# Kernel tuning notes

Measured on AMD Instinct MI355X. Metric: run time of the kernel, lower is better.

## Reference

```python
import jax, jax.numpy as jnp
import numpy as np

G = 7          # grid size
OBJ_P = 0.3    # fraction of cells containing an object


def _to_xyxy(x, y, w, h, m, n):
    # x pairs with grid index m (dim 2), y with n (dim 3), per the original loop
    cx = (x + m) / G
    cy = (y + n) / G
    return cx - w / 2, cy - h / 2, cx + w / 2, cy + h / 2


def _iou(b1, b2):
    x1a, y1a, x2a, y2a = b1
    x1b, y1b, x2b, y2b = b2
    iw = jnp.maximum(jnp.minimum(x2a, x2b) - jnp.maximum(x1a, x1b), 0.0)
    ih = jnp.maximum(jnp.minimum(y2a, y2b) - jnp.maximum(y1a, y1b), 0.0)
    inter = iw * ih
    a1 = (x2a - x1a) * (y2a - y1a)
    a2 = (x2b - x1b) * (y2b - y1b)
    union = a1 + a2 - inter
    return jnp.where(inter > 0, inter / union, 0.0)


def setup_inputs() -> dict:
    key = jax.random.key(0)
    k1, k2, k3 = jax.random.split(key, 3)
    B = 32768
    pred = jax.random.uniform(k1, (B, 30, G, G), dtype=jnp.float32)
    labels = jax.random.uniform(k2, (B, 30, G, G), dtype=jnp.float32)
    obj_mask = jax.random.bernoulli(k3, OBJ_P, (B, G, G)).astype(jnp.float32)
    labels = labels.at[:, 4].set(obj_mask)
    return {"pred": pred, "labels": labels}


def reference(pred, labels):
    B = pred.shape[0]
    m = jnp.arange(G, dtype=pred.dtype)[:, None]   # dim 2
    n = jnp.arange(G, dtype=pred.dtype)[None, :]   # dim 3

    obj = labels[:, 4] == 1.0                       # (B,G,G)

    box1 = _to_xyxy(pred[:, 0], pred[:, 1], pred[:, 2], pred[:, 3], m, n)
    box2 = _to_xyxy(pred[:, 5], pred[:, 6], pred[:, 7], pred[:, 8], m, n)
    boxg = _to_xyxy(labels[:, 0], labels[:, 1], labels[:, 2], labels[:, 3], m, n)

    iou1 = _iou(box1, boxg)
    iou2 = _iou(box2, boxg)
    resp1 = iou1 >= iou2

    coor1 = 5.0 * (jnp.sum((pred[:, 0:2] - labels[:, 0:2]) ** 2, axis=1)
                   + jnp.sum((jnp.sqrt(pred[:, 2:4]) - jnp.sqrt(labels[:, 2:4])) ** 2, axis=1))
    coor2 = 5.0 * (jnp.sum((pred[:, 5:7] - labels[:, 5:7]) ** 2, axis=1)
                   + jnp.sum((jnp.sqrt(pred[:, 7:9]) - jnp.sqrt(labels[:, 7:9])) ** 2, axis=1))

    loss_b1 = coor1 + (pred[:, 4] - iou1) ** 2 + 0.5 * (pred[:, 9] - iou2) ** 2
    loss_b2 = coor2 + (pred[:, 9] - iou2) ** 2 + 0.5 * (pred[:, 4] - iou1) ** 2

    cls = jnp.sum((pred[:, 10:] - labels[:, 10:]) ** 2, axis=1)

    obj_loss = jnp.where(resp1, loss_b1, loss_b2) + cls
    noobj_loss = 0.5 * (pred[:, 4] ** 2 + pred[:, 9] ** 2)

    total = jnp.sum(jnp.where(obj, obj_loss, noobj_loss))
    return total / B
```

## Files before the change

kernel.cpp:

```cpp
#include <hip/hip_runtime.h>


#define GRID 7
#define NCH 30
#define CPI (GRID * GRID)
#define FPI (NCH * CPI)
#define IPB 4
#define BLK 256
#define CELLS_PB (IPB * CPI)
#define F_PB (IPB * FPI)
#define F4_PB (F_PB / 4)
#define FALLBACK_NBLK 2048

typedef const __attribute__((address_space(1))) void gvoid_t;
typedef __attribute__((address_space(3))) void lvoid_t;

__device__ __forceinline__ float iou_xyxy(float x1a, float y1a, float x2a, float y2a,
                                          float x1b, float y1b, float x2b, float y2b) {
    float iw = fmaxf(fminf(x2a, x2b) - fmaxf(x1a, x1b), 0.0f);
    float ih = fmaxf(fminf(y2a, y2b) - fmaxf(y1a, y1b), 0.0f);
    float inter = iw * ih;
    float a1 = (x2a - x1a) * (y2a - y1a);
    float a2 = (x2b - x1b) * (y2b - y1b);
    float uni = a1 + a2 - inter;
    return inter > 0.0f ? inter / uni : 0.0f;
}

__device__ __forceinline__ float cell_loss(const float* __restrict__ pb,
                                           const float* __restrict__ lb,
                                           float fm, float fn) {
    float p0 = pb[0 * CPI], p1 = pb[1 * CPI], p2 = pb[2 * CPI], p3 = pb[3 * CPI];
    float p4 = pb[4 * CPI], p5 = pb[5 * CPI], p6 = pb[6 * CPI], p7 = pb[7 * CPI];
    float p8 = pb[8 * CPI], p9 = pb[9 * CPI];
    float l0 = lb[0 * CPI], l1 = lb[1 * CPI], l2 = lb[2 * CPI], l3 = lb[3 * CPI];
    float lobj = lb[4 * CPI];
    float l5 = lb[5 * CPI], l6 = lb[6 * CPI], l7 = lb[7 * CPI], l8 = lb[8 * CPI];

    float cls = 0.0f;
    #pragma unroll
    for (int c = 10; c < NCH; ++c) {
        float d = pb[c * CPI] - lb[c * CPI];
        cls += d * d;
    }

    const float inv_g = 1.0f / (float)GRID;

    float cx = (p0 + fm) * inv_g, cy = (p1 + fn) * inv_g;
    float b1x1 = cx - p2 * 0.5f, b1y1 = cy - p3 * 0.5f;
    float b1x2 = cx + p2 * 0.5f, b1y2 = cy + p3 * 0.5f;
    cx = (p5 + fm) * inv_g; cy = (p6 + fn) * inv_g;
    float b2x1 = cx - p7 * 0.5f, b2y1 = cy - p8 * 0.5f;
    float b2x2 = cx + p7 * 0.5f, b2y2 = cy + p8 * 0.5f;
    cx = (l0 + fm) * inv_g; cy = (l1 + fn) * inv_g;
    float gx1 = cx - l2 * 0.5f, gy1 = cy - l3 * 0.5f;
    float gx2 = cx + l2 * 0.5f, gy2 = cy + l3 * 0.5f;

    float iou1 = iou_xyxy(b1x1, b1y1, b1x2, b1y2, gx1, gy1, gx2, gy2);
    float iou2 = iou_xyxy(b2x1, b2y1, b2x2, b2y2, gx1, gy1, gx2, gy2);
    bool resp1 = iou1 >= iou2;

    float dx = p0 - l0, dy = p1 - l1;
    float dw = sqrtf(p2) - sqrtf(l2), dh = sqrtf(p3) - sqrtf(l3);
    float coor1 = 5.0f * (dx * dx + dy * dy + dw * dw + dh * dh);
    dx = p5 - l5; dy = p6 - l6;
    dw = sqrtf(p7) - sqrtf(l7); dh = sqrtf(p8) - sqrtf(l8);
    float coor2 = 5.0f * (dx * dx + dy * dy + dw * dw + dh * dh);

    float e1 = p4 - iou1, e2 = p9 - iou2;
    float loss_b1 = coor1 + e1 * e1 + 0.5f * e2 * e2;
    float loss_b2 = coor2 + e2 * e2 + 0.5f * e1 * e1;

    float obj_loss = (resp1 ? loss_b1 : loss_b2) + cls;
    float noobj_loss = 0.5f * (p4 * p4 + p9 * p9);

    return (lobj == 1.0f) ? obj_loss : noobj_loss;
}

__global__ void __launch_bounds__(BLK) yolo_partial_kernel(
        const float* __restrict__ pred,
        const float* __restrict__ labels,
        float* __restrict__ partials,
        int ngroups, float invB) {
    __shared__ __align__(16) float sp[F_PB];
    __shared__ __align__(16) float sl[F_PB];

    float acc = 0.0f;

    for (int g = blockIdx.x; g < ngroups; g += gridDim.x) {
        const float* gp = pred   + (size_t)g * F_PB;
        const float* gl = labels + (size_t)g * F_PB;

        for (int j = threadIdx.x; j < F4_PB; j += BLK)
            __builtin_amdgcn_global_load_lds((gvoid_t*)(gp + 4 * j),
                                             (lvoid_t*)(sp + 4 * j), 16, 0, 0);
        for (int j = threadIdx.x; j < F4_PB; j += BLK)
            __builtin_amdgcn_global_load_lds((gvoid_t*)(gl + 4 * j),
                                             (lvoid_t*)(sl + 4 * j), 16, 0, 0);

        asm volatile("s_waitcnt vmcnt(0)" ::: "memory");
        __syncthreads();

        int t = threadIdx.x;
        if (t < CELLS_PB) {
            int i = t / CPI;
            int cell = t - i * CPI;
            int m = cell / GRID;
            int n = cell - m * GRID;
            acc += cell_loss(&sp[i * FPI + cell], &sl[i * FPI + cell],
                             (float)m, (float)n) * invB;
        }
        __syncthreads();
    }

    #pragma unroll
    for (int off = 32; off > 0; off >>= 1)
        acc += __shfl_down(acc, off, 64);

    __shared__ float rsm[4];
    int lane = threadIdx.x & 63;
    int wid = threadIdx.x >> 6;
    if (lane == 0) rsm[wid] = acc;
    __syncthreads();
    if (threadIdx.x == 0)
        partials[blockIdx.x] = rsm[0] + rsm[1] + rsm[2] + rsm[3];
}

__global__ void __launch_bounds__(256) yolo_final_kernel(
        const float* __restrict__ partials, int np,
        const float* __restrict__ pred, const float* __restrict__ labels,
        int b0, int B, float invB, float* __restrict__ out) {
    float acc = 0.0f;
    for (int i = threadIdx.x; i < np; i += 256)
        acc += partials[i];

    int remcells = (B - b0) * CPI;
    for (int idx = threadIdx.x; idx < remcells; idx += 256) {
        int b = b0 + idx / CPI;
        int cell = idx % CPI;
        int m = cell / GRID;
        int n = cell - m * GRID;
        acc += cell_loss(pred + (size_t)b * FPI + cell,
                         labels + (size_t)b * FPI + cell,
                         (float)m, (float)n) * invB;
    }

    #pragma unroll
    for (int off = 32; off > 0; off >>= 1)
        acc += __shfl_down(acc, off, 64);
    __shared__ float rsm[4];
    int lane = threadIdx.x & 63;
    int wid = threadIdx.x >> 6;
    if (lane == 0) rsm[wid] = acc;
    __syncthreads();
    if (threadIdx.x == 0)
        out[0] = rsm[0] + rsm[1] + rsm[2] + rsm[3];
}

extern "C" void kernel_launch(void* const* d_in, const int* in_sizes, int n_in,
                              void* d_out, int out_size, void* d_ws, size_t ws_size,
                              hipStream_t stream) {
    const float* pred = (const float*)d_in[0];
    const float* labels = (const float*)d_in[1];
    float* out = (float*)d_out;
    float* partials = (float*)d_ws;

    int total = in_sizes[0];
    int B = total / FPI;
    if (B <= 0) return;
    float invB = 1.0f / (float)B;
    int ngroups = B / IPB;
    int b0 = ngroups * IPB;

    int nblk = ngroups;
    if (ngroups == 0) {
        nblk = 1;
    } else if ((size_t)ngroups * sizeof(float) > ws_size) {
        nblk = (ngroups < FALLBACK_NBLK) ? ngroups : FALLBACK_NBLK;
    }

    yolo_partial_kernel<<<nblk, BLK, 0, stream>>>(pred, labels, partials,
                                                  ngroups, invB);
    yolo_final_kernel<<<1, 256, 0, stream>>>(partials, nblk, pred, labels,
                                             b0, B, invB, out);
}
```

Measured before the change: 379.8 us.

## Double-buffer LDS staging with persistent grid to overlap loads and compute

Switches from one block per 4-image group to a persistent grid of 768 blocks, each processing 2-image groups and prefetching the next group into a second LDS buffer while computing the current one. Uses explicit vmcnt waits and raw s_barrier so the next group's loads stay in flight across the compute phase. The goal is to hide global-memory latency and avoid the full drain before every group. In exchange it raises LDS use per block, which may limit occupancy, and relies on a hand-counted vmcnt value.

Result: no change. 382.5 us (+0.7%).

```diff
diff --git a/kernel.cpp b/kernel.cpp
--- a/kernel.cpp
+++ b/kernel.cpp
@@ -5,12 +5,14 @@
 #define NCH 30
 #define CPI (GRID * GRID)
 #define FPI (NCH * CPI)
-#define IPB 4
+#define IPB 2
 #define BLK 256
 #define CELLS_PB (IPB * CPI)
 #define F_PB (IPB * FPI)
 #define F4_PB (F_PB / 4)
-#define FALLBACK_NBLK 2048
+#define ITERS 3
+#define PAD_F (ITERS * BLK * 4)
+#define NBLK 768
 
 typedef const __attribute__((address_space(1))) void gvoid_t;
 typedef __attribute__((address_space(3))) void lvoid_t;
@@ -76,29 +78,45 @@
     return (lobj == 1.0f) ? obj_loss : noobj_loss;
 }
 
+__device__ __forceinline__ void stage(const float* __restrict__ gsrc, float* lds) {
+    #pragma unroll
+    for (int it = 0; it < ITERS; ++it) {
+        int j = threadIdx.x + it * BLK;
+        int jc = (j < F4_PB) ? j : (F4_PB - 1);
+        __builtin_amdgcn_global_load_lds((gvoid_t*)(gsrc + 4 * jc),
+                                         (lvoid_t*)(lds + 4 * j), 16, 0, 0);
+    }
+}
+
 __global__ void __launch_bounds__(BLK) yolo_partial_kernel(
         const float* __restrict__ pred,
         const float* __restrict__ labels,
         float* __restrict__ partials,
         int ngroups, float invB) {
-    __shared__ __align__(16) float sp[F_PB];
-    __shared__ __align__(16) float sl[F_PB];
+    __shared__ __align__(16) float sp[2][PAD_F];
+    __shared__ __align__(16) float sl[2][PAD_F];
 
     float acc = 0.0f;
-
-    for (int g = blockIdx.x; g < ngroups; g += gridDim.x) {
-        const float* gp = pred   + (size_t)g * F_PB;
-        const float* gl = labels + (size_t)g * F_PB;
-
-        for (int j = threadIdx.x; j < F4_PB; j += BLK)
-            __builtin_amdgcn_global_load_lds((gvoid_t*)(gp + 4 * j),
-                                             (lvoid_t*)(sp + 4 * j), 16, 0, 0);
-        for (int j = threadIdx.x; j < F4_PB; j += BLK)
-            __builtin_amdgcn_global_load_lds((gvoid_t*)(gl + 4 * j),
-                                             (lvoid_t*)(sl + 4 * j), 16, 0, 0);
-
-        asm volatile("s_waitcnt vmcnt(0)" ::: "memory");
-        __syncthreads();
+    int step = gridDim.x;
+    int g0 = blockIdx.x;
+    int cur = 0;
+
+    if (g0 < ngroups) {
+        stage(pred   + (size_t)g0 * F_PB, sp[0]);
+        stage(labels + (size_t)g0 * F_PB, sl[0]);
+    }
+
+    for (int g = g0; g < ngroups; g += step) {
+        int gn = g + step;
+        if (gn < ngroups) {
+            stage(pred   + (size_t)gn * F_PB, sp[cur ^ 1]);
+            stage(labels + (size_t)gn * F_PB, sl[cur ^ 1]);
+            asm volatile("s_waitcnt vmcnt(6)" ::: "memory");
+        } else {
+            asm volatile("s_waitcnt vmcnt(0)" ::: "memory");
+        }
+        __builtin_amdgcn_sched_barrier(0);
+        __builtin_amdgcn_s_barrier();
 
         int t = threadIdx.x;
         if (t < CELLS_PB) {
@@ -106,11 +124,15 @@
             int cell = t - i * CPI;
             int m = cell / GRID;
             int n = cell - m * GRID;
-            acc += cell_loss(&sp[i * FPI + cell], &sl[i * FPI + cell],
+            acc += cell_loss(&sp[cur][i * FPI + cell], &sl[cur][i * FPI + cell],
                              (float)m, (float)n) * invB;
         }
-        __syncthreads();
-    }
+        asm volatile("s_waitcnt lgkmcnt(0)" ::: "memory");
+        __builtin_amdgcn_sched_barrier(0);
+        __builtin_amdgcn_s_barrier();
+        cur ^= 1;
+    }
+    asm volatile("s_waitcnt vmcnt(0)" ::: "memory");
 
     #pragma unroll
     for (int off = 32; off > 0; off >>= 1)
@@ -171,12 +193,9 @@
     int ngroups = B / IPB;
     int b0 = ngroups * IPB;
 
-    int nblk = ngroups;
-    if (ngroups == 0) {
-        nblk = 1;
-    } else if ((size_t)ngroups * sizeof(float) > ws_size) {
-        nblk = (ngroups < FALLBACK_NBLK) ? ngroups : FALLBACK_NBLK;
-    }
+    int nblk = (ngroups < NBLK) ? (ngroups > 0 ? ngroups : 1) : NBLK;
+    if ((size_t)nblk * sizeof(float) > ws_size)
+        nblk = (int)(ws_size / sizeof(float)) > 0 ? (int)(ws_size / sizeof(float)) : 1;
 
     yolo_partial_kernel<<<nblk, BLK, 0, stream>>>(pred, labels, partials,
                                                   ngroups, invB);
```
